# Performance work log

Measured on AMD Instinct MI355X. Metric: run time of the kernel, lower is better.

Reference implementation:

```python
import jax, jax.numpy as jnp
import numpy as np

CUTOFF = 3.0   # self.cutoff
RMIN = 3.5     # rmin in cutoff_function (note rmin > cutoff, faithful to source)
ETA = 4.0
N_RADIAL = 5
N_3BODY = 12
NATOMS = 2048
K = 48         # neighbors per atom (equal counts -> ragged loop becomes dense batch)
HID = 64
NPAIRS = NATOMS * K


def setup_inputs() -> dict:
    key = jax.random.key(0)
    ks = jax.random.split(key, 4)
    # displacements scaled so |rij| is mostly within a few Angstrom
    rij = jax.random.normal(ks[0], (NPAIRS, 3), jnp.float32) * 1.5
    # sorted-by-atom pair list with K neighbors per atom
    unique_i = jnp.repeat(jnp.arange(NATOMS, dtype=jnp.int64), K)
    W1 = jax.random.normal(ks[1], (N_RADIAL + N_3BODY, HID), jnp.float32) * 0.1
    b1 = jnp.zeros((HID,), jnp.float32)
    W2 = jax.random.normal(ks[2], (HID, HID), jnp.float32) * 0.1
    b2 = jnp.zeros((HID,), jnp.float32)
    W3 = jax.random.normal(ks[3], (HID, 1), jnp.float32) * 0.1
    b3 = jnp.zeros((1,), jnp.float32)
    return dict(rij=rij, unique_i=unique_i, W1=W1, b1=b1, W2=W2, b2=b2, W3=W3, b3=b3)


def _energy(rij, W1, b1, W2, b2, W3, b3):
    d = jnp.linalg.norm(rij, axis=1, keepdims=True)           # (P,1)
    diff_norm = rij / jnp.maximum(d, 1e-12)                   # F.normalize
    # pair cutoff (rmin=3.5, c=3.0 as in source)
    fc = jnp.where(d > RMIN,
                   0.5 + 0.5 * jnp.cos(jnp.pi * (d - RMIN) / (CUTOFF - RMIN)),
                   1.0)
    # radial Bessel basis, n = 1..5
    ns = jnp.arange(1, N_RADIAL + 1, dtype=rij.dtype)
    rbf = jnp.sqrt(2.0 / CUTOFF) * jnp.sin(ns * jnp.pi / CUTOFF * d) / d * fc  # (P,5)
    # 3-body Gaussian descriptors
    fcrik = (0.5 + 0.5 * jnp.cos(jnp.pi * d / CUTOFF))[:, 0]  # (P,)
    dn = diff_norm.reshape(NATOMS, K, 3)
    cosang = jnp.einsum('nkd,nld->nkl', dn, dn)               # (N,K,K) pairwise mm
    cosang = jnp.where(jnp.eye(K, dtype=bool)[None], 0.0, cosang)  # fill_diagonal_(0)
    mu = jnp.linspace(-1.0, 1.0, N_3BODY).astype(rij.dtype)
    w = fcrik.reshape(NATOMS, 1, K, 1)                        # fcrik broadcast on axis being summed
    g3b = jnp.sum(jnp.exp(-ETA * (cosang[..., None] - mu) ** 2) * w, axis=2)  # (N,K,12)
    g3b = g3b.reshape(NPAIRS, N_3BODY)
    desc = jnp.concatenate([rbf, g3b], axis=1)                # (P,17)
    h = jnp.tanh(desc @ W1 + b1)
    h = jnp.tanh(h @ W2 + b2)
    eij = h @ W3 + b3                                         # (P,1)
    return jnp.sum(eij * fc)


def reference(rij, unique_i, W1, b1, W2, b2, W3, b3):
    # Module output: gradients of total energy w.r.t. rij (written into beta)
    return jax.grad(_energy)(rij, W1, b1, W2, b2, W3, b3)
```

## Files before the change

### kernel.cpp

```cpp
#include <hip/hip_runtime.h>
#include <hip/hip_bf16.h>

#define NATOMS 2048
#define K 48
#define P (NATOMS * K)
#define NR 5
#define NM 12
#define ND 17
#define HID 64

#define PI_F 3.14159265358979f
#define CUT 3.0f
#define RMIN_F 3.5f
#define AFC (-6.28318530717959f)
#define POC (PI_F / CUT)
#define SQ 0.816496580927726f
#define E1C 1.45454545454545f
#define CMC (-0.132231404958678f)
#define N4L (-5.77078016355585f)
#define E1L (2.09846551402031f)
#define TL2 (2.88539008177793f)

__device__ unsigned short g_w1t[64 * 32];
__device__ unsigned short g_w2t[64 * 64];
__device__ unsigned short g_w2r[64 * 64];
__device__ unsigned short g_w1r[32 * 64];

using frag_ab = __attribute__((ext_vector_type(8))) short;
using frag_cd = __attribute__((ext_vector_type(4))) float;
using f2 = __attribute__((ext_vector_type(2))) float;
using f4 = __attribute__((ext_vector_type(4))) float;

__device__ __forceinline__ float fast_tanh(float x) {
    const float t = __builtin_amdgcn_exp2f(TL2 * x);
    return 1.0f - 2.0f * __builtin_amdgcn_rcpf(t + 1.0f);
}

__device__ __forceinline__ unsigned short f2bs(float x) {
    __hip_bfloat16 b = __float2bfloat16(x);
    return __builtin_bit_cast(unsigned short, b);
}

__device__ __forceinline__ float bs2f(unsigned short u) {
    return __builtin_bit_cast(float, ((unsigned)u) << 16);
}

__global__ __launch_bounds__(256) void k_prep(const float* __restrict__ W1,
                                              const float* __restrict__ W2) {
    const int i = blockIdx.x * 256 + threadIdx.x;
    if (i < 2048) {
        const int n = i >> 5, k = i & 31;
        g_w1t[i] = (k < ND) ? f2bs(W1[k * HID + n]) : (unsigned short)0;
    } else if (i < 2048 + 4096) {
        const int j = i - 2048, n = j >> 6, k = j & 63;
        g_w2t[j] = f2bs(W2[k * HID + n]);
    } else if (i < 2048 + 8192) {
        const int j = i - (2048 + 4096);
        g_w2r[j] = f2bs(W2[j]);
    } else if (i < 2048 + 8192 + 2048) {
        const int j = i - (2048 + 8192), n = j >> 6;
        g_w1r[j] = (n < ND) ? f2bs(W1[j]) : (unsigned short)0;
    }
}

#define H1_OFF   0
#define ST_OFF   0
#define DESC_OFF 6912
#define GZ2_OFF  6912
#define SGD_OFF  6912
#define SGF_OFF  10560
#define SGU_OFF  11328
#define SS_OFF   13824
#define SE_OFF   18528
#define SU_OFF   19296
#define SFC_OFF  20064
#define SFK_OFF  20256
#define SM_BYTES 20448

__global__ __launch_bounds__(256, 8) void k_fused(const float* __restrict__ rij,
                                                  const float* __restrict__ b1,
                                                  const float* __restrict__ b2,
                                                  const float* __restrict__ W3,
                                                  const float* __restrict__ b3,
                                                  float* __restrict__ out) {
    __shared__ __align__(16) char smem[SM_BYTES];
    short*          h1S   = (short*)(smem + H1_OFF);
    unsigned short* sT    = (unsigned short*)(smem + ST_OFF);
    short*          descS = (short*)(smem + DESC_OFF);
    short*          gz2S  = (short*)(smem + GZ2_OFF);
    float*          sgd   = (float*)(smem + SGD_OFF);
    float*          sgf4  = (float*)(smem + SGF_OFF);
    float*          sgu4  = (float*)(smem + SGU_OFF);
    unsigned short* sS    = (unsigned short*)(smem + SS_OFF);
    float*          se    = (float*)(smem + SE_OFF);
    float*          su    = (float*)(smem + SU_OFF);
    float*          sfc   = (float*)(smem + SFC_OFF);
    float*          sfk   = (float*)(smem + SFK_OFF);

    const int t = threadIdx.x;
    const int base3 = blockIdx.x * (K * 3);

    if (t < K) {
        const float x = rij[base3 + 3 * t];
        const float y = rij[base3 + 3 * t + 1];
        const float z = rij[base3 + 3 * t + 2];
        float s2 = fmaxf(x * x + y * y + z * z, 1e-24f);
        const float inv = __builtin_amdgcn_rsqf(s2);
        const float d = s2 * inv;
        *(f4*)&su[4 * t] = (f4){x * inv, y * inv, z * inv, d};
        sfk[t] = 0.5f + 0.5f * __cosf(POC * d);
        sfc[t] = (d > RMIN_F) ? (0.5f + 0.5f * __cosf(AFC * (d - RMIN_F))) : 1.0f;
#pragma unroll
        for (int c = ND; c < 32; c++) descS[t * 40 + c] = 0;
    }
    __syncthreads();

    if (t < 192) {
        const int k = t >> 2, ch = t & 3;
        const f4 uk = *(const f4*)&su[4 * k];
        const float* sul = &su[4 * (ch * 12)];
        f2 partv[6];
#pragma unroll
        for (int i = 0; i < 6; i++) partv[i] = (f2){0.0f, 0.0f};
#pragma unroll
        for (int li = 0; li < 12; li++) {
            const int l = ch * 12 + li;
            const f4 ul = *(const f4*)&sul[4 * li];
            float c = uk.x * ul.x + uk.y * ul.y + uk.z * ul.z;
            if (k == l) c = 0.0f;
            const float cp1 = c + 1.0f;
            const float e0 = __builtin_amdgcn_exp2f(N4L * cp1 * cp1) * sfk[l];
            const float e1 = __builtin_amdgcn_exp2f(E1L * cp1);
            const float e2s = e1 * e1;
            const f2 e2v = {e2s, e2s};
            f2 tm = {e0, e0 * e1};
            partv[0] += tm;
#pragma unroll
            for (int i = 1; i < 6; i++) { tm *= e2v; partv[i] += tm; }
        }
#pragma unroll
        for (int i = 0; i < 6; i++) {
            partv[i].x += __shfl_xor(partv[i].x, 1);
            partv[i].y += __shfl_xor(partv[i].y, 1);
            partv[i].x += __shfl_xor(partv[i].x, 2);
            partv[i].y += __shfl_xor(partv[i].y, 2);
        }
        if (ch == 0) {
#pragma unroll
            for (int i = 0; i < 6; i++) {
                const int m0 = 2 * i, m1 = 2 * i + 1;
                descS[k * 40 + NR + m0] =
                    (short)f2bs(partv[i].x * __expf(CMC * (float)(m0 * m0)));
                descS[k * 40 + NR + m1] =
                    (short)f2bs(partv[i].y * __expf(CMC * (float)(m1 * m1)));
            }
        }
    } else {
#pragma unroll
        for (int r = 0; r < 4; r++) {
            const int idx = (t - 192) + 64 * r;
            if (idx < K * NR) {
                const int p = idx / NR, n = idx - NR * p;
                const float d = su[4 * p + 3];
                const float s = SQ * sfc[p] * __builtin_amdgcn_rcpf(d);
                descS[p * 40 + n] = (short)f2bs(s * __sinf((float)(n + 1) * POC * d));
            }
        }
    }
    __syncthreads();

    const int w = t >> 6, lane = t & 63, quad = lane >> 4, lm = lane & 15;
    const int n0 = w * 16 + lm;

    float t1[3][4];
    {
        const frag_ab bf = *(const frag_ab*)&g_w1t[n0 * 32 + quad * 8];
        const float bias = b1[n0];
#pragma unroll
        for (int mt = 0; mt < 3; mt++) {
            const frag_ab a = *(const frag_ab*)&descS[(mt * 16 + lm) * 40 + quad * 8];
            frag_cd acc = {bias, bias, bias, bias};
            acc = __builtin_amdgcn_mfma_f32_16x16x32_bf16(a, bf, acc, 0, 0, 0);
#pragma unroll
            for (int r = 0; r < 4; r++) {
                const float tv = fast_tanh(acc[r]);
                t1[mt][r] = tv;
                h1S[(mt * 16 + quad * 4 + r) * 72 + n0] = (short)f2bs(tv);
            }
        }
    }
    __syncthreads();

    {
        const frag_ab b0 = *(const frag_ab*)&g_w2t[n0 * 64 + quad * 8];
        const frag_ab b1f = *(const frag_ab*)&g_w2t[n0 * 64 + 32 + quad * 8];
        const float bias = b2[n0];
        const float w3n = W3[n0];
#pragma unroll
        for (int mt = 0; mt < 3; mt++) {
            const frag_ab a0 = *(const frag_ab*)&h1S[(mt * 16 + lm) * 72 + quad * 8];
            const frag_ab a1 = *(const frag_ab*)&h1S[(mt * 16 + lm) * 72 + 32 + quad * 8];
            frag_cd acc = {bias, bias, bias, bias};
            acc = __builtin_amdgcn_mfma_f32_16x16x32_bf16(a0, b0, acc, 0, 0, 0);
            acc = __builtin_amdgcn_mfma_f32_16x16x32_bf16(a1, b1f, acc, 0, 0, 0);
            float ep[4];
#pragma unroll
            for (int r = 0; r < 4; r++) {
                const int row = mt * 16 + quad * 4 + r;
                const float tv = fast_tanh(acc[r]);
                ep[r] = tv * w3n;
                gz2S[row * 72 + n0] = (short)f2bs(sfc[row] * w3n * (1.0f - tv * tv));
            }
#pragma unroll
            for (int off = 1; off < 16; off <<= 1) {
#pragma unroll
                for (int r = 0; r < 4; r++) ep[r] += __shfl_xor(ep[r], off, 64);
            }
            if (lm == 0) {
#pragma unroll
                for (int r = 0; r < 4; r++) se[w * 48 + mt * 16 + quad * 4 + r] = ep[r];
            }
        }
    }
    __syncthreads();

    {
        const frag_ab b0 = *(const frag_ab*)&g_w2r[n0 * 64 + quad * 8];
        const frag_ab b1f = *(const frag_ab*)&g_w2r[n0 * 64 + 32 + quad * 8];
#pragma unroll
        for (int mt = 0; mt < 3; mt++) {
            const frag_ab a0 = *(const frag_ab*)&gz2S[(mt * 16 + lm) * 72 + quad * 8];
            const frag_ab a1 = *(const frag_ab*)&gz2S[(mt * 16 + lm) * 72 + 32 + quad * 8];
            frag_cd acc = {0.0f, 0.0f, 0.0f, 0.0f};
            acc = __builtin_amdgcn_mfma_f32_16x16x32_bf16(a0, b0, acc, 0, 0, 0);
            acc = __builtin_amdgcn_mfma_f32_16x16x32_bf16(a1, b1f, acc, 0, 0, 0);
#pragma unroll
            for (int r = 0; r < 4; r++) {
                const float g = acc[r] * (1.0f - t1[mt][r] * t1[mt][r]);
                h1S[(mt * 16 + quad * 4 + r) * 72 + n0] = (short)f2bs(g);
            }
        }
    }
    __syncthreads();

    for (int tid = w; tid < 6; tid += 4) {
        const int mt = tid >> 1, nt = tid & 1, n = nt * 16 + lm;
        const frag_ab b0 = *(const frag_ab*)&g_w1r[n * 64 + quad * 8];
        const frag_ab b1f = *(const frag_ab*)&g_w1r[n * 64 + 32 + quad * 8];
        const frag_ab a0 = *(const frag_ab*)&h1S[(mt * 16 + lm) * 72 + quad * 8];
        const frag_ab a1 = *(const frag_ab*)&h1S[(mt * 16 + lm) * 72 + 32 + quad * 8];
        frag_cd acc = {0.0f, 0.0f, 0.0f, 0.0f};
        acc = __builtin_amdgcn_mfma_f32_16x16x32_bf16(a0, b0, acc, 0, 0, 0);
        acc = __builtin_amdgcn_mfma_f32_16x16x32_bf16(a1, b1f, acc, 0, 0, 0);
        if (n < ND) {
            const int mm = n - NR;
            const float cmul = (n >= NR) ? __expf(CMC * (float)(mm * mm)) : 1.0f;
#pragma unroll
            for (int r = 0; r < 4; r++)
                sgd[(mt * 16 + quad * 4 + r) * 19 + n] = acc[r] * cmul;
        }
    }
    if (t < K)
        sgd[t * 19 + 17] = se[t] + se[48 + t] + se[96 + t] + se[144 + t] + b3[0];
    __syncthreads();

    if (t < 192) {
        const int k = t >> 2, ch = t & 3;
        f2 gm[NM];
#pragma unroll
        for (int m = 0; m < NM; m++) {
            const float g = sgd[k * 19 + NR + m];
            gm[m] = (f2){g, (float)m * g};
        }
        const f4 uk = *(const f4*)&su[4 * k];
        const float* sul = &su[4 * (ch * 12)];
#pragma unroll
        for (int li = 0; li < 12; li++) {
            const int l = ch * 12 + li;
            const f4 ul = *(const f4*)&sul[4 * li];
            float c = uk.x * ul.x + uk.y * ul.y + uk.z * ul.z;
            if (k == l) c = 0.0f;
            const float cp1 = c + 1.0f;
            const float e0 = __builtin_amdgcn_exp2f(N4L * cp1 * cp1);
            const float x = __builtin_amdgcn_exp2f(E1L * cp1);
            const f2 xx = {x, x};
            f2 pd = gm[11];
#pragma unroll
            for (int m = 10; m >= 1; m--) pd = __builtin_elementwise_fma(pd, xx, gm[m]);
            const float Pv = fmaf(pd.x, x, gm[0].x);
            const float T = e0 * Pv;
            const float U = e0 * x * pd.y;
            const float Sp = fmaf(cp1, T, -(2.0f / 11.0f) * U);
            const float Sv = (k == l) ? 0.0f : (-8.0f) * Sp;
            sT[k * 49 + l] = f2bs(T);
            sS[k * 49 + l] = f2bs(Sv);
        }
    }
    __syncthreads();

    if (lane < K) {
        float s = 0.0f;
#pragma unroll
        for (int kk = 12 * w; kk < 12 * w + 12; kk++) s += bs2f(sT[kk * 49 + lane]);
        sgf4[w * 48 + lane] = s;

        const int k = lane;
        const float fk = sfk[k];
        float gx = 0.0f, gy = 0.0f, gz = 0.0f;
#pragma unroll
        for (int l = 12 * w; l < 12 * w + 12; l++) {
            const float wgt = fmaf(bs2f(sS[k * 49 + l]), sfk[l],
                                   bs2f(sS[l * 49 + k]) * fk);
            const f4 ul = *(const f4*)&su[4 * l];
            gx = fmaf(wgt, ul.x, gx);
            gy = fmaf(wgt, ul.y, gy);
            gz = fmaf(wgt, ul.z, gz);
        }
        sgu4[(w * 48 + k) * 3 + 0] = gx;
        sgu4[(w * 48 + k) * 3 + 1] = gy;
        sgu4[(w * 48 + k) * 3 + 2] = gz;
    }
    __syncthreads();

    if (t < K) {
        const float sgf_t = sgf4[t] + sgf4[48 + t] + sgf4[96 + t] + sgf4[144 + t];
        float gux = 0.0f, guy = 0.0f, guz = 0.0f;
#pragma unroll
        for (int ww = 0; ww < 4; ww++) {
            gux += sgu4[(ww * 48 + t) * 3 + 0];
            guy += sgu4[(ww * 48 + t) * 3 + 1];
            guz += sgu4[(ww * 48 + t) * 3 + 2];
        }
        const f4 uv = *(const f4*)&su[4 * t];
        const float d = uv.w;
        const float ux = uv.x, uy = uv.y, uz = uv.z;
        const float invd = __builtin_amdgcn_rcpf(d);
        float gfc = sgd[t * 19 + 17];
        float gdR = 0.0f;
#pragma unroll
        for (int n = 0; n < NR; n++) {
            const float bn = (float)(n + 1) * POC;
            float sn, cn;
            __sincosf(bn * d, &sn, &cn);
            const float g = sgd[t * 19 + n];
            gfc = fmaf(g, SQ * sn * invd, gfc);
            gdR = fmaf(g, SQ * (bn * cn - sn * invd) * invd, gdR);
        }
        const float fc = sfc[t];
        float dfc = 0.0f;
        if (d > RMIN_F) dfc = -0.5f * AFC * __sinf(AFC * (d - RMIN_F));
        const float dfcrik = -0.5f * POC * __sinf(POC * d);

        const float gd = fc * gdR + gfc * dfc + sgf_t * dfcrik;
        const float dot = gux * ux + guy * uy + guz * uz;

        out[base3 + 3 * t + 0] = fmaf(gd, ux, (gux - dot * ux) * invd);
        out[base3 + 3 * t + 1] = fmaf(gd, uy, (guy - dot * uy) * invd);
        out[base3 + 3 * t + 2] = fmaf(gd, uz, (guz - dot * uz) * invd);
    }
}

extern "C" void kernel_launch(void* const* d_in, const int* in_sizes, int n_in,
                              void* d_out, int out_size, void* d_ws, size_t ws_size,
                              hipStream_t stream) {
    (void)in_sizes; (void)n_in; (void)out_size; (void)d_ws; (void)ws_size;
    const float* rij = (const float*)d_in[0];
    const float* W1 = (const float*)d_in[2];
    const float* b1 = (const float*)d_in[3];
    const float* W2 = (const float*)d_in[4];
    const float* b2 = (const float*)d_in[5];
    const float* W3 = (const float*)d_in[6];
    const float* b3 = (const float*)d_in[7];
    float* out = (float*)d_out;

    k_prep<<<48, 256, 0, stream>>>(W1, W2);
    k_fused<<<NATOMS, 256, 0, stream>>>(rij, b1, b2, W3, b3, out);
}
```

Baseline: 92.63 us.

## Hoist weight fragment loads to kernel start and use DPP reductions

Moves the per-wave loads of W1/W2 bf16 MFMA fragments, biases and W3 to the start of the kernel so their global latency overlaps the descriptor computation. Replaces __shfl_xor reductions with DPP quad-permute and row-shift adds, vectorises sfk/sfc shared reads into f4 loads, and lowers launch_bounds occupancy from 8 to 6 blocks per CU to make room for the extra live registers. The trade is fewer resident waves to hide latency, in exchange for earlier loads and cheaper cross-lane reductions.

```diff
diff --git a/kernel.cpp b/kernel.cpp
--- a/kernel.cpp
+++ b/kernel.cpp
@@ -43,6 +43,13 @@
 
 __device__ __forceinline__ float bs2f(unsigned short u) {
     return __builtin_bit_cast(float, ((unsigned)u) << 16);
+}
+
+template <int CTRL>
+__device__ __forceinline__ float dpp_add(float x) {
+    const int y = __builtin_amdgcn_update_dpp(
+        0, __builtin_bit_cast(int, x), CTRL, 0xF, 0xF, true);
+    return x + __builtin_bit_cast(float, y);
 }
 
 __global__ __launch_bounds__(256) void k_prep(const float* __restrict__ W1,
@@ -77,7 +84,7 @@
 #define SFK_OFF  20256
 #define SM_BYTES 20448
 
-__global__ __launch_bounds__(256, 8) void k_fused(const float* __restrict__ rij,
+__global__ __launch_bounds__(256, 6) void k_fused(const float* __restrict__ rij,
                                                   const float* __restrict__ b1,
                                                   const float* __restrict__ b2,
                                                   const float* __restrict__ W3,
@@ -99,6 +106,18 @@
 
     const int t = threadIdx.x;
     const int base3 = blockIdx.x * (K * 3);
+    const int w = t >> 6, lane = t & 63, quad = lane >> 4, lm = lane & 15;
+    const int n0 = w * 16 + lm;
+
+    const frag_ab wf1  = *(const frag_ab*)&g_w1t[n0 * 32 + quad * 8];
+    const frag_ab wf2a = *(const frag_ab*)&g_w2t[n0 * 64 + quad * 8];
+    const frag_ab wf2b = *(const frag_ab*)&g_w2t[n0 * 64 + 32 + quad * 8];
+    const frag_ab wr2a = *(const frag_ab*)&g_w2r[n0 * 64 + quad * 8];
+    const frag_ab wr2b = *(const frag_ab*)&g_w2r[n0 * 64 + 32 + quad * 8];
+    const float bias1 = b1[n0];
+    const float bias2 = b2[n0];
+    const float w3n   = W3[n0];
+    const float b3v   = b3[0];
 
     if (t < K) {
         const float x = rij[base3 + 3 * t];
@@ -119,6 +138,10 @@
         const int k = t >> 2, ch = t & 3;
         const f4 uk = *(const f4*)&su[4 * k];
         const float* sul = &su[4 * (ch * 12)];
+        f4 fkq[3];
+        fkq[0] = *(const f4*)&sfk[ch * 12];
+        fkq[1] = *(const f4*)&sfk[ch * 12 + 4];
+        fkq[2] = *(const f4*)&sfk[ch * 12 + 8];
         f2 partv[6];
 #pragma unroll
         for (int i = 0; i < 6; i++) partv[i] = (f2){0.0f, 0.0f};
@@ -129,7 +152,7 @@
             float c = uk.x * ul.x + uk.y * ul.y + uk.z * ul.z;
             if (k == l) c = 0.0f;
             const float cp1 = c + 1.0f;
-            const float e0 = __builtin_amdgcn_exp2f(N4L * cp1 * cp1) * sfk[l];
+            const float e0 = __builtin_amdgcn_exp2f(N4L * cp1 * cp1) * fkq[li >> 2][li & 3];
             const float e1 = __builtin_amdgcn_exp2f(E1L * cp1);
             const float e2s = e1 * e1;
             const f2 e2v = {e2s, e2s};
@@ -140,10 +163,8 @@
         }
 #pragma unroll
         for (int i = 0; i < 6; i++) {
-            partv[i].x += __shfl_xor(partv[i].x, 1);
-            partv[i].y += __shfl_xor(partv[i].y, 1);
-            partv[i].x += __shfl_xor(partv[i].x, 2);
-            partv[i].y += __shfl_xor(partv[i].y, 2);
+            partv[i].x = dpp_add<0x4E>(dpp_add<0xB1>(partv[i].x));
+            partv[i].y = dpp_add<0x4E>(dpp_add<0xB1>(partv[i].y));
         }
         if (ch == 0) {
 #pragma unroll
@@ -169,18 +190,13 @@
     }
     __syncthreads();
 
-    const int w = t >> 6, lane = t & 63, quad = lane >> 4, lm = lane & 15;
-    const int n0 = w * 16 + lm;
-
     float t1[3][4];
     {
-        const frag_ab bf = *(const frag_ab*)&g_w1t[n0 * 32 + quad * 8];
-        const float bias = b1[n0];
 #pragma unroll
         for (int mt = 0; mt < 3; mt++) {
             const frag_ab a = *(const frag_ab*)&descS[(mt * 16 + lm) * 40 + quad * 8];
-            frag_cd acc = {bias, bias, bias, bias};
-            acc = __builtin_amdgcn_mfma_f32_16x16x32_bf16(a, bf, acc, 0, 0, 0);
+            frag_cd acc = {bias1, bias1, bias1, bias1};
+            acc = __builtin_amdgcn_mfma_f32_16x16x32_bf16(a, wf1, acc, 0, 0, 0);
 #pragma unroll
             for (int r = 0; r < 4; r++) {
                 const float tv = fast_tanh(acc[r]);
@@ -192,31 +208,26 @@
     __syncthreads();
 
     {
-        const frag_ab b0 = *(const frag_ab*)&g_w2t[n0 * 64 + quad * 8];
-        const frag_ab b1f = *(const frag_ab*)&g_w2t[n0 * 64 + 32 + quad * 8];
-        const float bias = b2[n0];
-        const float w3n = W3[n0];
 #pragma unroll
         for (int mt = 0; mt < 3; mt++) {
             const frag_ab a0 = *(const frag_ab*)&h1S[(mt * 16 + lm) * 72 + quad * 8];
             const frag_ab a1 = *(const frag_ab*)&h1S[(mt * 16 + lm) * 72 + 32 + quad * 8];
-            frag_cd acc = {bias, bias, bias, bias};
-            acc = __builtin_amdgcn_mfma_f32_16x16x32_bf16(a0, b0, acc, 0, 0, 0);
-            acc = __builtin_amdgcn_mfma_f32_16x16x32_bf16(a1, b1f, acc, 0, 0, 0);
+            frag_cd acc = {bias2, bias2, bias2, bias2};
+            acc = __builtin_amdgcn_mfma_f32_16x16x32_bf16(a0, wf2a, acc, 0, 0, 0);
+            acc = __builtin_amdgcn_mfma_f32_16x16x32_bf16(a1, wf2b, acc, 0, 0, 0);
+            const f4 fcv = *(const f4*)&sfc[mt * 16 + quad * 4];
             float ep[4];
 #pragma unroll
             for (int r = 0; r < 4; r++) {
                 const int row = mt * 16 + quad * 4 + r;
                 const float tv = fast_tanh(acc[r]);
                 ep[r] = tv * w3n;
-                gz2S[row * 72 + n0] = (short)f2bs(sfc[row] * w3n * (1.0f - tv * tv));
-            }
-#pragma unroll
-            for (int off = 1; off < 16; off <<= 1) {
-#pragma unroll
-                for (int r = 0; r < 4; r++) ep[r] += __shfl_xor(ep[r], off, 64);
-            }
-            if (lm == 0) {
+                gz2S[row * 72 + n0] = (short)f2bs(fcv[r] * w3n * (1.0f - tv * tv));
+            }
+#pragma unroll
+            for (int r = 0; r < 4; r++)
+                ep[r] = dpp_add<0x118>(dpp_add<0x114>(dpp_add<0x112>(dpp_add<0x111>(ep[r]))));
+            if (lm == 15) {
 #pragma unroll
                 for (int r = 0; r < 4; r++) se[w * 48 + mt * 16 + quad * 4 + r] = ep[r];
             }
@@ -225,15 +236,13 @@
     __syncthreads();
 
     {
-        const frag_ab b0 = *(const frag_ab*)&g_w2r[n0 * 64 + quad * 8];
-        const frag_ab b1f = *(const frag_ab*)&g_w2r[n0 * 64 + 32 + quad * 8];
 #pragma unroll
         for (int mt = 0; mt < 3; mt++) {
             const frag_ab a0 = *(const frag_ab*)&gz2S[(mt * 16 + lm) * 72 + quad * 8];
             const frag_ab a1 = *(const frag_ab*)&gz2S[(mt * 16 + lm) * 72 + 32 + quad * 8];
             frag_cd acc = {0.0f, 0.0f, 0.0f, 0.0f};
-            acc = __builtin_amdgcn_mfma_f32_16x16x32_bf16(a0, b0, acc, 0, 0, 0);
-            acc = __builtin_amdgcn_mfma_f32_16x16x32_bf16(a1, b1f, acc, 0, 0, 0);
+            acc = __builtin_amdgcn_mfma_f32_16x16x32_bf16(a0, wr2a, acc, 0, 0, 0);
+            acc = __builtin_amdgcn_mfma_f32_16x16x32_bf16(a1, wr2b, acc, 0, 0, 0);
 #pragma unroll
             for (int r = 0; r < 4; r++) {
                 const float g = acc[r] * (1.0f - t1[mt][r] * t1[mt][r]);
@@ -261,7 +270,7 @@
         }
     }
     if (t < K)
-        sgd[t * 19 + 17] = se[t] + se[48 + t] + se[96 + t] + se[144 + t] + b3[0];
+        sgd[t * 19 + 17] = se[t] + se[48 + t] + se[96 + t] + se[144 + t] + b3v;
     __syncthreads();
 
     if (t < 192) {
```

After: 93.52 us. No clear change (+1.0%).
